# Kernel tuning notes

Measured on AMD Instinct MI355X. Metric: run time of the kernel, lower is better.

The kernel has to match this reference:

```python
import jax, jax.numpy as jnp
import numpy as np

B, S, E, H = 2, 2048, 2048, 16
HD = E // H  # head_dim = 128


def setup_inputs() -> dict:
    key = jax.random.key(0)
    ks = jax.random.split(key, 7)
    inp = {
        "query": jax.random.normal(ks[0], (B, S, E), dtype=jnp.float32),
        "key": jax.random.normal(ks[1], (B, S, E), dtype=jnp.float32),
        "value": jax.random.normal(ks[2], (B, S, E), dtype=jnp.float32),
        # qkv: Linear(E, 3E) -> weight [3E, E], bias [3E]
        "Wqkv": jax.random.normal(ks[3], (3 * E, E), dtype=jnp.float32) * (E ** -0.5),
        "bqkv": jnp.zeros((3 * E,), dtype=jnp.float32),
        # proj: Linear(E, E) (source bug-fixed; see notes)
        "Wproj": jax.random.normal(ks[4], (E, E), dtype=jnp.float32) * (E ** -0.5),
        "bproj": jnp.zeros((E,), dtype=jnp.float32),
    }
    return inp


def reference(query, key, value, Wqkv, bqkv, Wproj, bproj):
    # NB: `key` and `value` are unused by the original forward.
    b, s, _ = query.shape
    qkv = query @ Wqkv.T + bqkv                      # [B, S, 3E]
    qkv = qkv.reshape(b, s, H, 3 * HD).transpose(0, 2, 1, 3)  # [B, H, S, 3*HD]
    q = qkv[..., :HD]
    k = qkv[..., HD:2 * HD]
    v = qkv[..., 2 * HD:]
    # Source divides by scale_factor = HD**-0.5, i.e. MULTIPLIES by sqrt(HD).
    scores = jnp.einsum("bhqd,bhkd->bhqk", q, k) * (HD ** 0.5)
    attn = jax.nn.softmax(scores, axis=-1)           # dropout p=0 -> identity
    out = jnp.einsum("bhqk,bhkd->bhqd", attn, v)     # [B, H, S, HD]
    out = out.transpose(0, 2, 1, 3).reshape(b, s, E)  # [B, S, E]
    return out @ Wproj.T + bproj
```

## Files before the change

kernel.cpp:

```cpp
#include <hip/hip_runtime.h>

#define B_  2
#define S_  2048
#define E_  2048
#define H_  16
#define HD_ 128
#define M_  (B_*S_)
#define N1_ (3*E_)
#define K_  E_

typedef _Float16 f16;
typedef __attribute__((ext_vector_type(8))) _Float16 f16x8;
typedef __attribute__((ext_vector_type(4))) _Float16 f16x4;
typedef __attribute__((ext_vector_type(4))) float    f32x4;
typedef __attribute__((ext_vector_type(4))) float    fv4;

__global__ void cvt_f32_f16(const float* __restrict__ src, f16* __restrict__ dst, int n4) {
    int i = blockIdx.x * blockDim.x + threadIdx.x;
    if (i < n4) {
        fv4 v = ((const fv4*)src)[i];
        f16x4 h;
        h.x = (f16)v.x; h.y = (f16)v.y; h.z = (f16)v.z; h.w = (f16)v.w;
        ((f16x4*)dst)[i] = h;
    }
}

__device__ __forceinline__ int swz8(int row, int g) {
    return row * 64 + ((g ^ (row & 7)) << 3);
}
__device__ __forceinline__ int swz16(int row, int g) {
    return row * 128 + ((g ^ (row & 15)) << 3);
}

__device__ __forceinline__ void split8(fv4 a0, fv4 a1, float scale, f16x8& hi, f16x8& lo) {
    float x[8] = {a0.x, a0.y, a0.z, a0.w, a1.x, a1.y, a1.z, a1.w};
#pragma unroll
    for (int e = 0; e < 8; ++e) {
        float xs = x[e] * scale;
        f16 h = (f16)xs;
        hi[e] = h;
        lo[e] = (f16)(xs - (float)h);
    }
}

__global__ __launch_bounds__(256) void gemm_qkv(
    const float* __restrict__ A, const float* __restrict__ W, const float* __restrict__ bias,
    f16* __restrict__ qh, f16* __restrict__ kh, f16* __restrict__ vT)
{
    __shared__ f16 As_hi[128 * 64];
    __shared__ f16 As_lo[128 * 64];
    __shared__ f16 Bs_hi[128 * 64];
    __shared__ f16 Bs_lo[128 * 64];
    const int t = threadIdx.x;
    const int w = t >> 6, lane = t & 63, quad = lane >> 4, l15 = lane & 15;
    const int m0 = blockIdx.y * 128, n0 = blockIdx.x * 128;
    const int wm = (w & 1) * 64, wn = (w >> 1) * 64;
    const int tile_part = (n0 % 384) >> 7;
    const bool need_lo = (tile_part != 2);

    f32x4 acc[4][4];
#pragma unroll
    for (int i = 0; i < 4; ++i)
#pragma unroll
        for (int j = 0; j < 4; ++j) { acc[i][j].x = 0.f; acc[i][j].y = 0.f; acc[i][j].z = 0.f; acc[i][j].w = 0.f; }

    for (int kb = 0; kb < K_ / 64; ++kb) {
        const float* Ag = A + (size_t)m0 * K_ + kb * 64;
        const float* Bg = W + (size_t)n0 * K_ + kb * 64;
#pragma unroll
        for (int i = 0; i < 4; ++i) {
            int gid = t + i * 256;
            int row = gid >> 3, g = gid & 7;
            const float* ap = Ag + (size_t)row * K_ + g * 8;
            fv4 a0 = *(const fv4*)ap;
            fv4 a1 = *(const fv4*)(ap + 4);
            f16x8 hi, lo;
            split8(a0, a1, 1.0f, hi, lo);
            *(f16x8*)&As_hi[swz8(row, g)] = hi;
            *(f16x8*)&As_lo[swz8(row, g)] = lo;
            const float* bp = Bg + (size_t)row * K_ + g * 8;
            fv4 b0 = *(const fv4*)bp;
            fv4 b1 = *(const fv4*)(bp + 4);
            split8(b0, b1, 64.0f, hi, lo);
            *(f16x8*)&Bs_hi[swz8(row, g)] = hi;
            *(f16x8*)&Bs_lo[swz8(row, g)] = lo;
        }
        __syncthreads();
#pragma unroll
        for (int ks = 0; ks < 2; ++ks) {
            f16x8 ah[4], al[4], bh[4], bl[4];
            int g = ks * 4 + quad;
#pragma unroll
            for (int mt = 0; mt < 4; ++mt) {
                int row = wm + mt * 16 + l15;
                ah[mt] = *(const f16x8*)&As_hi[swz8(row, g)];
                al[mt] = *(const f16x8*)&As_lo[swz8(row, g)];
            }
#pragma unroll
            for (int nt = 0; nt < 4; ++nt) {
                int row = wn + nt * 16 + l15;
                bh[nt] = *(const f16x8*)&Bs_hi[swz8(row, g)];
                bl[nt] = *(const f16x8*)&Bs_lo[swz8(row, g)];
            }
#pragma unroll
            for (int mt = 0; mt < 4; ++mt)
#pragma unroll
                for (int nt = 0; nt < 4; ++nt) {
                    acc[mt][nt] = __builtin_amdgcn_mfma_f32_16x16x32_f16(ah[mt], bh[nt], acc[mt][nt], 0, 0, 0);
                    if (need_lo) {
                        acc[mt][nt] = __builtin_amdgcn_mfma_f32_16x16x32_f16(ah[mt], bl[nt], acc[mt][nt], 0, 0, 0);
                        acc[mt][nt] = __builtin_amdgcn_mfma_f32_16x16x32_f16(al[mt], bh[nt], acc[mt][nt], 0, 0, 0);
                    }
                }
        }
        __syncthreads();
    }

    const float inv_s = 1.0f / 64.0f;
#pragma unroll
    for (int nt = 0; nt < 4; ++nt) {
        int n = n0 + wn + nt * 16 + l15;
        float bs = bias[n];
        int h = n / 384;
        int r = n % 384;
        int part = r >> 7;
        int d = r & 127;
#pragma unroll
        for (int mt = 0; mt < 4; ++mt) {
            int mbase = m0 + wm + mt * 16 + quad * 4;
            int b = mbase >> 11, s = mbase & 2047;
            int bh = b * H_ + h;
            if (part == 2) {
                f16x4 pv;
                pv.x = (f16)(acc[mt][nt].x * inv_s + bs);
                pv.y = (f16)(acc[mt][nt].y * inv_s + bs);
                pv.z = (f16)(acc[mt][nt].z * inv_s + bs);
                pv.w = (f16)(acc[mt][nt].w * inv_s + bs);
                *(f16x4*)&vT[((size_t)bh * 128 + d) * 2048 + s] = pv;
            } else {
                f16* dst = (part == 0) ? qh : kh;
                size_t base = (size_t)bh * 2048 * 128;
#pragma unroll
                for (int reg = 0; reg < 4; ++reg)
                    dst[base + (size_t)(s + reg) * 128 + d] = (f16)(acc[mt][nt][reg] * inv_s + bs);
            }
        }
    }
}

__global__ __launch_bounds__(256) void attn(
    const f16* __restrict__ qh, const f16* __restrict__ kh, const f16* __restrict__ vT,
    f16* __restrict__ ao)
{
    __shared__ f16 Ks[128 * 128];
    __shared__ f16 Vts[128 * 128];
    const int t = threadIdx.x;
    const int w = t >> 6, lane = t & 63, quad = lane >> 4, l15 = lane & 15;
    const int bh = blockIdx.y;
    const int q0 = blockIdx.x * 128;
    const f16* Q  = qh + (size_t)bh * 2048 * 128;
    const f16* Kp = kh + (size_t)bh * 2048 * 128;
    const f16* Vp = vT + (size_t)bh * 128 * 2048;

    const float C2 = (float)(11.313708498984761 * 1.4426950408889634);

    f16x8 qf[2][4];
#pragma unroll
    for (int mt = 0; mt < 2; ++mt)
#pragma unroll
        for (int ks = 0; ks < 4; ++ks) {
            int row = q0 + w * 32 + mt * 16 + l15;
            qf[mt][ks] = *(const f16x8*)&Q[(size_t)row * 128 + ks * 32 + quad * 8];
        }

    f32x4 o[2][8];
    float mrow[2][4], lrow[2][4];
#pragma unroll
    for (int mt = 0; mt < 2; ++mt) {
#pragma unroll
        for (int dt = 0; dt < 8; ++dt) { o[mt][dt].x = 0.f; o[mt][dt].y = 0.f; o[mt][dt].z = 0.f; o[mt][dt].w = 0.f; }
#pragma unroll
        for (int reg = 0; reg < 4; ++reg) { mrow[mt][reg] = -1e30f; lrow[mt][reg] = 0.f; }
    }

    for (int j = 0; j < 16; ++j) {
        __syncthreads();
#pragma unroll
        for (int i = 0; i < 8; ++i) {
            int c = t + i * 256;
            int row = c >> 4, g = c & 15;
            *(f16x8*)&Ks[swz16(row, g)]  = *(const f16x8*)&Kp[(size_t)(j * 128 + row) * 128 + g * 8];
            *(f16x8*)&Vts[swz16(row, g)] = *(const f16x8*)&Vp[(size_t)row * 2048 + j * 128 + g * 8];
        }
        __syncthreads();

        f32x4 sa[2][8];
#pragma unroll
        for (int mt = 0; mt < 2; ++mt)
#pragma unroll
            for (int nt = 0; nt < 8; ++nt) { sa[mt][nt].x = 0.f; sa[mt][nt].y = 0.f; sa[mt][nt].z = 0.f; sa[mt][nt].w = 0.f; }
#pragma unroll
        for (int ks = 0; ks < 4; ++ks) {
            int g = ks * 4 + quad;
            f16x8 bf[8];
#pragma unroll
            for (int nt = 0; nt < 8; ++nt) { int row = nt * 16 + l15; bf[nt] = *(const f16x8*)&Ks[swz16(row, g)]; }
#pragma unroll
            for (int mt = 0; mt < 2; ++mt)
#pragma unroll
                for (int nt = 0; nt < 8; ++nt)
                    sa[mt][nt] = __builtin_amdgcn_mfma_f32_16x16x32_f16(qf[mt][ks], bf[nt], sa[mt][nt], 0, 0, 0);
        }

        float mnew[2][4], alpha[2][4];
#pragma unroll
        for (int mt = 0; mt < 2; ++mt)
#pragma unroll
            for (int reg = 0; reg < 4; ++reg) {
                float mx = sa[mt][0][reg];
#pragma unroll
                for (int nt = 1; nt < 8; ++nt) mx = fmaxf(mx, sa[mt][nt][reg]);
                mx *= C2;
#pragma unroll
                for (int d = 1; d < 16; d <<= 1) mx = fmaxf(mx, __shfl_xor(mx, d));
                float mn = fmaxf(mrow[mt][reg], mx);
                mnew[mt][reg]  = mn;
                alpha[mt][reg] = exp2f(mrow[mt][reg] - mn);
                mrow[mt][reg]  = mn;
            }
#pragma unroll
        for (int mt = 0; mt < 2; ++mt)
#pragma unroll
            for (int reg = 0; reg < 4; ++reg) {
                float rs = 0.f;
#pragma unroll
                for (int nt = 0; nt < 8; ++nt) {
                    float p = exp2f(sa[mt][nt][reg] * C2 - mnew[mt][reg]);
                    sa[mt][nt][reg] = p;
                    rs += p;
                }
#pragma unroll
                for (int d = 1; d < 16; d <<= 1) rs += __shfl_xor(rs, d);
                lrow[mt][reg] = lrow[mt][reg] * alpha[mt][reg] + rs;
#pragma unroll
                for (int dt = 0; dt < 8; ++dt) o[mt][dt][reg] *= alpha[mt][reg];
            }

        __syncthreads();
#pragma unroll
        for (int mt = 0; mt < 2; ++mt)
#pragma unroll
            for (int nt = 0; nt < 8; ++nt) {
                int col = nt * 16 + l15;
#pragma unroll
                for (int reg = 0; reg < 4; ++reg) {
                    int row = w * 32 + mt * 16 + quad * 4 + reg;
                    Ks[row * 128 + (((col >> 3) ^ (row & 15)) << 3) + (col & 7)] = (f16)sa[mt][nt][reg];
                }
            }
        __syncthreads();

#pragma unroll
        for (int ks = 0; ks < 4; ++ks) {
            int g = ks * 4 + quad;
            f16x8 pf[2], vf[8];
#pragma unroll
            for (int mt = 0; mt < 2; ++mt) { int row = w * 32 + mt * 16 + l15; pf[mt] = *(const f16x8*)&Ks[swz16(row, g)]; }
#pragma unroll
            for (int dt = 0; dt < 8; ++dt) { int row = dt * 16 + l15; vf[dt] = *(const f16x8*)&Vts[swz16(row, g)]; }
#pragma unroll
            for (int mt = 0; mt < 2; ++mt)
#pragma unroll
                for (int dt = 0; dt < 8; ++dt)
                    o[mt][dt] = __builtin_amdgcn_mfma_f32_16x16x32_f16(pf[mt], vf[dt], o[mt][dt], 0, 0, 0);
        }
    }

    const int b = bh >> 4, h = bh & 15;
#pragma unroll
    for (int mt = 0; mt < 2; ++mt) {
        float inv[4];
#pragma unroll
        for (int reg = 0; reg < 4; ++reg) inv[reg] = 1.0f / lrow[mt][reg];
#pragma unroll
        for (int dt = 0; dt < 8; ++dt) {
            int col = h * 128 + dt * 16 + l15;
#pragma unroll
            for (int reg = 0; reg < 4; ++reg) {
                int srow = q0 + w * 32 + mt * 16 + quad * 4 + reg;
                ao[(size_t)((b << 11) + srow) * 2048 + col] = (f16)(o[mt][dt][reg] * inv[reg]);
            }
        }
    }
}

__global__ __launch_bounds__(256) void gemm_proj(
    const f16* __restrict__ A, const f16* __restrict__ W, const float* __restrict__ bias,
    float* __restrict__ out)
{
    __shared__ f16 As[128 * 64];
    __shared__ f16 Bs[128 * 64];
    const int t = threadIdx.x;
    const int w = t >> 6, lane = t & 63, quad = lane >> 4, l15 = lane & 15;
    const int m0 = blockIdx.y * 128, n0 = blockIdx.x * 128;
    const int wm = (w & 1) * 64, wn = (w >> 1) * 64;

    f32x4 acc[4][4];
#pragma unroll
    for (int i = 0; i < 4; ++i)
#pragma unroll
        for (int j = 0; j < 4; ++j) { acc[i][j].x = 0.f; acc[i][j].y = 0.f; acc[i][j].z = 0.f; acc[i][j].w = 0.f; }

    for (int kb = 0; kb < K_ / 64; ++kb) {
        const f16* Ag = A + (size_t)m0 * K_ + kb * 64;
        const f16* Bg = W + (size_t)n0 * K_ + kb * 64;
#pragma unroll
        for (int i = 0; i < 4; ++i) {
            int c = t + i * 256;
            int row = c >> 3, g = c & 7;
            *(f16x8*)&As[swz8(row, g)] = *(const f16x8*)(Ag + (size_t)row * K_ + g * 8);
            *(f16x8*)&Bs[swz8(row, g)] = *(const f16x8*)(Bg + (size_t)row * K_ + g * 8);
        }
        __syncthreads();
#pragma unroll
        for (int ks = 0; ks < 2; ++ks) {
            f16x8 af[4], bf[4];
            int g = ks * 4 + quad;
#pragma unroll
            for (int mt = 0; mt < 4; ++mt) { int row = wm + mt * 16 + l15; af[mt] = *(const f16x8*)&As[swz8(row, g)]; }
#pragma unroll
            for (int nt = 0; nt < 4; ++nt) { int row = wn + nt * 16 + l15; bf[nt] = *(const f16x8*)&Bs[swz8(row, g)]; }
#pragma unroll
            for (int mt = 0; mt < 4; ++mt)
#pragma unroll
                for (int nt = 0; nt < 4; ++nt)
                    acc[mt][nt] = __builtin_amdgcn_mfma_f32_16x16x32_f16(af[mt], bf[nt], acc[mt][nt], 0, 0, 0);
        }
        __syncthreads();
    }

#pragma unroll
    for (int nt = 0; nt < 4; ++nt) {
        int n = n0 + wn + nt * 16 + l15;
        float bs = bias[n];
#pragma unroll
        for (int mt = 0; mt < 4; ++mt) {
            int mbase = m0 + wm + mt * 16 + quad * 4;
#pragma unroll
            for (int reg = 0; reg < 4; ++reg)
                out[(size_t)(mbase + reg) * 2048 + n] = acc[mt][nt][reg] + bs;
        }
    }
}

extern "C" void kernel_launch(void* const* d_in, const int* in_sizes, int n_in,
                              void* d_out, int out_size, void* d_ws, size_t ws_size,
                              hipStream_t stream) {
    const float* query = (const float*)d_in[0];
    const float* Wqkv  = (const float*)d_in[3];
    const float* bqkv  = (const float*)d_in[4];
    const float* Wproj = (const float*)d_in[5];
    const float* bproj = (const float*)d_in[6];
    float* out = (float*)d_out;

    char* ws = (char*)d_ws;
    const size_t MB = 1024ull * 1024ull;
    if (ws_size < 72 * MB) return;
    f16* w2  = (f16*)(ws);
    f16* qh  = (f16*)(ws + 8  * MB);
    f16* kh  = (f16*)(ws + 24 * MB);
    f16* vT  = (f16*)(ws + 40 * MB);
    f16* ao  = (f16*)(ws + 56 * MB);

    int n;
    n = E_ * E_ / 4;   cvt_f32_f16<<<(n + 255) / 256, 256, 0, stream>>>(Wproj, w2, n);

    gemm_qkv<<<dim3(N1_ / 128, M_ / 128), 256, 0, stream>>>(query, Wqkv, bqkv, qh, kh, vT);
    attn<<<dim3(S_ / 128, B_ * H_), 256, 0, stream>>>(qh, kh, vT, ao);
    gemm_proj<<<dim3(E_ / 128, M_ / 128), 256, 0, stream>>>(ao, w2, bproj, out);
}
```

Measured before the change: 673.2 us.

## Pre-split fp32 inputs to fp16 hi/lo and stage tiles with direct global-to-LDS loads

Adds a pre-pass that splits the query and the QKV weight into fp16 hi/lo arrays once, so the QKV GEMM no longer converts fp32 data inside its inner loop. The QKV GEMM, attention and projection kernels now fill swizzled shared-memory tiles with global_load_lds async copies instead of loads that pass through registers. The low-part loads for V-columns are skipped where they are not needed. In exchange it adds extra kernels and workspace traffic for the split arrays, and which path runs depends on the workspace size.

```diff
diff --git a/kernel.cpp b/kernel.cpp
--- a/kernel.cpp
+++ b/kernel.cpp
@@ -15,6 +15,65 @@
 typedef __attribute__((ext_vector_type(4))) float    f32x4;
 typedef __attribute__((ext_vector_type(4))) float    fv4;
 
+__device__ __forceinline__ void async16(const f16* g, f16* l) {
+    __builtin_amdgcn_global_load_lds(
+        (const __attribute__((address_space(1))) unsigned int*)g,
+        (__attribute__((address_space(3))) unsigned int*)l, 16, 0, 0);
+}
+
+__device__ __forceinline__ int swz8(int row, int g) {
+    return row * 64 + ((g ^ (row & 7)) << 3);
+}
+__device__ __forceinline__ int swz16(int row, int g) {
+    return row * 128 + ((g ^ (row & 15)) << 3);
+}
+
+__device__ __forceinline__ void stage_swz8(const f16* __restrict__ src, int ldg,
+                                           f16* lds, int w, int lane) {
+#pragma unroll
+    for (int i = 0; i < 4; ++i) {
+        int p = (w * 4 + i) * 64 + lane;
+        int row = p >> 3, gl = p & 7;
+        int gs = gl ^ (row & 7);
+        async16(src + (size_t)row * ldg + gs * 8, lds + (size_t)p * 8);
+    }
+}
+
+__device__ __forceinline__ void stage_swz16(const f16* __restrict__ src, int ldg,
+                                            f16* lds, int w, int lane) {
+#pragma unroll
+    for (int i = 0; i < 8; ++i) {
+        int p = (w * 8 + i) * 64 + lane;
+        int row = p >> 4, gl = p & 15;
+        int gs = gl ^ (row & 15);
+        async16(src + (size_t)row * ldg + gs * 8, lds + (size_t)p * 8);
+    }
+}
+
+__device__ __forceinline__ void split8(fv4 a0, fv4 a1, float scale, f16x8& hi, f16x8& lo) {
+    float x[8] = {a0.x, a0.y, a0.z, a0.w, a1.x, a1.y, a1.z, a1.w};
+#pragma unroll
+    for (int e = 0; e < 8; ++e) {
+        float xs = x[e] * scale;
+        f16 h = (f16)xs;
+        hi[e] = h;
+        lo[e] = (f16)(xs - (float)h);
+    }
+}
+
+__global__ void split_f32(const float* __restrict__ src, f16* __restrict__ hi,
+                          f16* __restrict__ lo, float scale, int n8) {
+    int i = blockIdx.x * blockDim.x + threadIdx.x;
+    if (i < n8) {
+        fv4 a0 = ((const fv4*)src)[2 * i];
+        fv4 a1 = ((const fv4*)src)[2 * i + 1];
+        f16x8 h, l;
+        split8(a0, a1, scale, h, l);
+        ((f16x8*)hi)[i] = h;
+        ((f16x8*)lo)[i] = l;
+    }
+}
+
 __global__ void cvt_f32_f16(const float* __restrict__ src, f16* __restrict__ dst, int n4) {
     int i = blockIdx.x * blockDim.x + threadIdx.x;
     if (i < n4) {
@@ -25,26 +84,10 @@
     }
 }
 
-__device__ __forceinline__ int swz8(int row, int g) {
-    return row * 64 + ((g ^ (row & 7)) << 3);
-}
-__device__ __forceinline__ int swz16(int row, int g) {
-    return row * 128 + ((g ^ (row & 15)) << 3);
-}
-
-__device__ __forceinline__ void split8(fv4 a0, fv4 a1, float scale, f16x8& hi, f16x8& lo) {
-    float x[8] = {a0.x, a0.y, a0.z, a0.w, a1.x, a1.y, a1.z, a1.w};
-#pragma unroll
-    for (int e = 0; e < 8; ++e) {
-        float xs = x[e] * scale;
-        f16 h = (f16)xs;
-        hi[e] = h;
-        lo[e] = (f16)(xs - (float)h);
-    }
-}
-
+template <bool AsyncA>
 __global__ __launch_bounds__(256) void gemm_qkv(
-    const float* __restrict__ A, const float* __restrict__ W, const float* __restrict__ bias,
+    const float* __restrict__ A, const f16* __restrict__ A_hi, const f16* __restrict__ A_lo,
+    const f16* __restrict__ W_hi, const f16* __restrict__ W_lo, const float* __restrict__ bias,
     f16* __restrict__ qh, f16* __restrict__ kh, f16* __restrict__ vT)
 {
     __shared__ f16 As_hi[128 * 64];
@@ -65,27 +108,30 @@
         for (int j = 0; j < 4; ++j) { acc[i][j].x = 0.f; acc[i][j].y = 0.f; acc[i][j].z = 0.f; acc[i][j].w = 0.f; }
 
     for (int kb = 0; kb < K_ / 64; ++kb) {
-        const float* Ag = A + (size_t)m0 * K_ + kb * 64;
-        const float* Bg = W + (size_t)n0 * K_ + kb * 64;
-#pragma unroll
-        for (int i = 0; i < 4; ++i) {
-            int gid = t + i * 256;
-            int row = gid >> 3, g = gid & 7;
-            const float* ap = Ag + (size_t)row * K_ + g * 8;
-            fv4 a0 = *(const fv4*)ap;
-            fv4 a1 = *(const fv4*)(ap + 4);
-            f16x8 hi, lo;
-            split8(a0, a1, 1.0f, hi, lo);
-            *(f16x8*)&As_hi[swz8(row, g)] = hi;
-            *(f16x8*)&As_lo[swz8(row, g)] = lo;
-            const float* bp = Bg + (size_t)row * K_ + g * 8;
-            fv4 b0 = *(const fv4*)bp;
-            fv4 b1 = *(const fv4*)(bp + 4);
-            split8(b0, b1, 64.0f, hi, lo);
-            *(f16x8*)&Bs_hi[swz8(row, g)] = hi;
-            *(f16x8*)&Bs_lo[swz8(row, g)] = lo;
-        }
-        __syncthreads();
+        stage_swz8(W_hi + (size_t)n0 * K_ + kb * 64, K_, Bs_hi, w, lane);
+        if (need_lo)
+            stage_swz8(W_lo + (size_t)n0 * K_ + kb * 64, K_, Bs_lo, w, lane);
+        if (AsyncA) {
+            stage_swz8(A_hi + (size_t)m0 * K_ + kb * 64, K_, As_hi, w, lane);
+            if (need_lo)
+                stage_swz8(A_lo + (size_t)m0 * K_ + kb * 64, K_, As_lo, w, lane);
+        } else {
+            const float* Ag = A + (size_t)m0 * K_ + kb * 64;
+#pragma unroll
+            for (int i = 0; i < 4; ++i) {
+                int gid = t + i * 256;
+                int row = gid >> 3, g = gid & 7;
+                const float* ap = Ag + (size_t)row * K_ + g * 8;
+                fv4 a0 = *(const fv4*)ap;
+                fv4 a1 = *(const fv4*)(ap + 4);
+                f16x8 hi, lo;
+                split8(a0, a1, 1.0f, hi, lo);
+                *(f16x8*)&As_hi[swz8(row, g)] = hi;
+                *(f16x8*)&As_lo[swz8(row, g)] = lo;
+            }
+        }
+        __syncthreads();
+
 #pragma unroll
         for (int ks = 0; ks < 2; ++ks) {
             f16x8 ah[4], al[4], bh[4], bl[4];
@@ -185,13 +231,8 @@
 
     for (int j = 0; j < 16; ++j) {
         __syncthreads();
-#pragma unroll
-        for (int i = 0; i < 8; ++i) {
-            int c = t + i * 256;
-            int row = c >> 4, g = c & 15;
-            *(f16x8*)&Ks[swz16(row, g)]  = *(const f16x8*)&Kp[(size_t)(j * 128 + row) * 128 + g * 8];
-            *(f16x8*)&Vts[swz16(row, g)] = *(const f16x8*)&Vp[(size_t)row * 2048 + j * 128 + g * 8];
-        }
+        stage_swz16(Kp + (size_t)(j * 128) * 128, 128, Ks, w, lane);
+        stage_swz16(Vp + j * 128, 2048, Vts, w, lane);
         __syncthreads();
 
         f32x4 sa[2][8];
@@ -312,15 +353,8 @@
         for (int j = 0; j < 4; ++j) { acc[i][j].x = 0.f; acc[i][j].y = 0.f; acc[i][j].z = 0.f; acc[i][j].w = 0.f; }
 
     for (int kb = 0; kb < K_ / 64; ++kb) {
-        const f16* Ag = A + (size_t)m0 * K_ + kb * 64;
-        const f16* Bg = W + (size_t)n0 * K_ + kb * 64;
-#pragma unroll
-        for (int i = 0; i < 4; ++i) {
-            int c = t + i * 256;
-            int row = c >> 3, g = c & 7;
-            *(f16x8*)&As[swz8(row, g)] = *(const f16x8*)(Ag + (size_t)row * K_ + g * 8);
-            *(f16x8*)&Bs[swz8(row, g)] = *(const f16x8*)(Bg + (size_t)row * K_ + g * 8);
-        }
+        stage_swz8(A + (size_t)m0 * K_ + kb * 64, K_, As, w, lane);
+        stage_swz8(W + (size_t)n0 * K_ + kb * 64, K_, Bs, w, lane);
         __syncthreads();
 #pragma unroll
         for (int ks = 0; ks < 2; ++ks) {
@@ -365,17 +399,42 @@
 
     char* ws = (char*)d_ws;
     const size_t MB = 1024ull * 1024ull;
-    if (ws_size < 72 * MB) return;
-    f16* w2  = (f16*)(ws);
-    f16* qh  = (f16*)(ws + 8  * MB);
-    f16* kh  = (f16*)(ws + 24 * MB);
-    f16* vT  = (f16*)(ws + 40 * MB);
-    f16* ao  = (f16*)(ws + 56 * MB);
-
-    int n;
-    n = E_ * E_ / 4;   cvt_f32_f16<<<(n + 255) / 256, 256, 0, stream>>>(Wproj, w2, n);
-
-    gemm_qkv<<<dim3(N1_ / 128, M_ / 128), 256, 0, stream>>>(query, Wqkv, bqkv, qh, kh, vT);
+    const bool big = (ws_size >= 128 * MB);
+
+    f16 *A_hi, *A_lo, *W_hi, *W_lo, *qh, *kh, *vT, *ao, *w2;
+    if (big) {
+        A_hi = (f16*)(ws);
+        A_lo = (f16*)(ws + 16 * MB);
+        W_hi = (f16*)(ws + 32 * MB);
+        W_lo = (f16*)(ws + 56 * MB);
+        qh   = (f16*)(ws + 80 * MB);
+        kh   = (f16*)(ws + 96 * MB);
+        vT   = (f16*)(ws + 112 * MB);
+        ao   = (f16*)(ws);
+        w2   = (f16*)(ws + 56 * MB);
+    } else {
+        if (ws_size < 96 * MB) return;
+        A_hi = A_lo = nullptr;
+        W_hi = (f16*)(ws);
+        W_lo = (f16*)(ws + 24 * MB);
+        qh   = (f16*)(ws + 48 * MB);
+        kh   = (f16*)(ws + 64 * MB);
+        vT   = (f16*)(ws + 80 * MB);
+        ao   = (f16*)(ws);
+        w2   = (f16*)(ws + 24 * MB);
+    }
+
+    if (big)
+        split_f32<<<(M_ * K_ / 8 + 255) / 256, 256, 0, stream>>>(query, A_hi, A_lo, 1.0f, M_ * K_ / 8);
+    split_f32<<<(N1_ * K_ / 8 + 255) / 256, 256, 0, stream>>>(Wqkv, W_hi, W_lo, 64.0f, N1_ * K_ / 8);
+
+    if (big)
+        gemm_qkv<true><<<dim3(N1_ / 128, M_ / 128), 256, 0, stream>>>(query, A_hi, A_lo, W_hi, W_lo, bqkv, qh, kh, vT);
+    else
+        gemm_qkv<false><<<dim3(N1_ / 128, M_ / 128), 256, 0, stream>>>(query, A_hi, A_lo, W_hi, W_lo, bqkv, qh, kh, vT);
+
+    cvt_f32_f16<<<(E_ * E_ / 4 + 255) / 256, 256, 0, stream>>>(Wproj, w2, E_ * E_ / 4);
+
     attn<<<dim3(S_ / 128, B_ * H_), 256, 0, stream>>>(qh, kh, vT, ao);
     gemm_proj<<<dim3(E_ / 128, M_ / 128), 256, 0, stream>>>(ao, w2, bproj, out);
 }
```

After: 639.5 us. -5.0%, faster.
